# Kernel optimization log

Measured on AMD Instinct MI355X. Metric: run time of the kernel, lower is better.

## Reference

```python
import jax, jax.numpy as jnp
import numpy as np

N, E, B = 50000, 800000, 64
IN, H, OUT = 64, 128, 64


def _gcn_norm(edge_index, num_nodes):
    # PyG gcn_norm with add_self_loops=True: A_hat = A + I, norm = d^-1/2[src]*d^-1/2[dst]
    loop = jnp.arange(num_nodes)
    src = jnp.concatenate([edge_index[0], loop])
    dst = jnp.concatenate([edge_index[1], loop])
    deg = jax.ops.segment_sum(jnp.ones_like(dst, dtype=jnp.float32), dst,
                              num_segments=num_nodes)  # >= 1 due to self-loops
    dis = deg ** -0.5
    norm = dis[src] * dis[dst]  # [E+N]
    return src, dst, norm


def _gcn_layer(x, W, b, src, dst, norm, num_nodes):
    h = x @ W                                   # linear first (GCNConv order)
    msg = h[src] * norm[:, None]                # gather + normalize, [E+N, H]
    out = jax.ops.segment_sum(msg, dst, num_segments=num_nodes)  # scatter-add
    return out + b


def setup_inputs() -> dict:
    key = jax.random.key(0)
    ks = jax.random.split(key, 12)
    x = jax.random.normal(ks[0], (N, IN), dtype=jnp.float32)
    edge_index = jax.random.randint(ks[1], (2, E), 0, N, dtype=jnp.int64)
    batch = jnp.sort(jax.random.randint(ks[2], (N,), 0, B, dtype=jnp.int64))

    def lin(k, fan_in, fan_out):
        s = 1.0 / np.sqrt(fan_in)
        return jax.random.uniform(k, (fan_in, fan_out), jnp.float32, -s, s)

    return {
        "x": x, "edge_index": edge_index, "batch": batch,
        "W1": lin(ks[3], IN, H), "b1": jnp.zeros((H,), jnp.float32),
        "W2": lin(ks[4], H, H),  "b2": jnp.zeros((H,), jnp.float32),
        "W3": lin(ks[5], H, H),  "b3": jnp.zeros((H,), jnp.float32),
        "W4": lin(ks[6], H, OUT), "b4": jnp.zeros((OUT,), jnp.float32),
    }


def reference(x, edge_index, batch, W1, b1, W2, b2, W3, b3, W4, b4):
    src, dst, norm = _gcn_norm(edge_index, N)
    h = jax.nn.relu(_gcn_layer(x, W1, b1, src, dst, norm, N))
    h = jax.nn.relu(_gcn_layer(h, W2, b2, src, dst, norm, N))
    # global mean pool over graphs
    sums = jax.ops.segment_sum(h, batch, num_segments=B)          # [B, H]
    cnts = jax.ops.segment_sum(jnp.ones((N,), jnp.float32), batch, num_segments=B)
    pooled = sums / jnp.maximum(cnts, 1.0)[:, None]
    # MLP head
    return jax.nn.relu(pooled @ W3 + b3) @ W4 + b4                # [B, OUT]
```

## Files before the change

kernel.cpp:

```cpp
#include <hip/hip_runtime.h>


__device__ __forceinline__ float ldf(const void* p, long long i, int f32) {
    if (f32) return ((const float*)p)[i];
    unsigned int u = ((const unsigned short*)p)[i];
    return __uint_as_float(u << 16);
}
__device__ __forceinline__ float bfl(unsigned int u) { return __uint_as_float(u << 16); }
__device__ __forceinline__ float bfh(unsigned int u) { return __uint_as_float(u & 0xFFFF0000u); }
__device__ __forceinline__ int ld_idx(const int* p, long long i, int i64) {
    return i64 ? p[2 * i] : p[i];
}
__device__ __forceinline__ unsigned short f2bf(float v) {
    unsigned int x = __float_as_uint(v);
    return (unsigned short)((x + 0x7FFFu + ((x >> 16) & 1u)) >> 16);
}
__device__ __forceinline__ int clampi(int v, int lo, int hi) {
    return v < lo ? lo : (v > hi ? hi : v);
}

#define OW1 0
#define OB1 8192
#define OW2 8320
#define OB2 24704
#define OW3 24832
#define OB3 41216
#define OW4 41344
#define OB4 49536
#define OTOT 49600


__global__ void gnn_prep(const void* W1, const void* b1, const void* W2, const void* b2,
                         const void* W3, const void* b3, const void* W4, const void* b4,
                         const void* x, const int* __restrict__ ei,
                         int* __restrict__ flags_out,
                         int* __restrict__ degcnt, float* __restrict__ pooled,
                         float* __restrict__ wsW, unsigned short* __restrict__ xb,
                         int N, int B) {
    __shared__ int s_cnt, s_or;
    const int t = threadIdx.x;
    if (t == 0) { s_cnt = 0; s_or = 0; }
    __syncthreads();
    {
        const unsigned int* w1w = (const unsigned int*)W1;
        int c = 0, o = 0;
        for (int i = t; i < 512; i += 256) {
            unsigned int e = (w1w[i] >> 7) & 0xFFu;
            if (e >= 100 && e <= 140) c++;
        }
        for (int i = t; i < 1024; i += 256) o |= ei[2 * i + 1];
        atomicAdd(&s_cnt, c);
        atomicOr(&s_or, o);
    }
    __syncthreads();
    const int f32 = (s_cnt > 256) ? 0 : 1;
    if (blockIdx.x == 0 && t == 0) {
        flags_out[0] = f32;
        flags_out[1] = (s_or == 0) ? 1 : 0;
    }
    const int i = blockIdx.x * 256 + t;
    const int stride = gridDim.x * 256;
    for (int j = i; j < N; j += stride) degcnt[j] = 0;
    for (int j = i; j < B * 128; j += stride) pooled[j] = 0.f;
    for (int j = i; j < OTOT; j += stride) {
        float v;
        if      (j < OB1) v = ldf(W1, j - OW1, f32);
        else if (j < OW2) v = ldf(b1, j - OB1, f32);
        else if (j < OB2) v = ldf(W2, j - OW2, f32);
        else if (j < OW3) v = ldf(b2, j - OB2, f32);
        else if (j < OB3) v = ldf(W3, j - OW3, f32);
        else if (j < OW4) v = ldf(b3, j - OB3, f32);
        else if (j < OB4) v = ldf(W4, j - OW4, f32);
        else              v = ldf(b4, j - OB4, f32);
        wsW[j] = v;
    }
    if (f32) {
        const float* xf = (const float*)x;
        for (int j = i; j < N * 64; j += stride) xb[j] = f2bf(xf[j]);
    }
}


__global__ void gnn_hist(const int* __restrict__ ei, int E, int N,
                         const int* __restrict__ flags, int* __restrict__ degcnt,
                         int* __restrict__ rank) {
    int base = (blockIdx.x * 256 + threadIdx.x) * 4;
    if (base >= E) return;
    int i64 = flags[1];
    int m = min(4, E - base);
    int d[4], r[4];
#pragma unroll
    for (int j = 0; j < 4; ++j)
        if (j < m) d[j] = clampi(ld_idx(ei, (long long)E + base + j, i64), 0, N - 1);
#pragma unroll
    for (int j = 0; j < 4; ++j)
        if (j < m) r[j] = atomicAdd(&degcnt[d[j]], 1);
#pragma unroll
    for (int j = 0; j < 4; ++j)
        if (j < m) rank[base + j] = r[j];
}

__global__ void gnn_scan1(const int* __restrict__ cnt, int* __restrict__ excl,
                          int* __restrict__ sums, float* __restrict__ dis, int N) {
    __shared__ int sh[256];
    int t = threadIdx.x;
    int i = blockIdx.x * 256 + t;
    int v = (i < N) ? cnt[i] : 0;
    sh[t] = v;
    __syncthreads();
    for (int off = 1; off < 256; off <<= 1) {
        int a = (t >= off) ? sh[t - off] : 0;
        __syncthreads();
        sh[t] += a;
        __syncthreads();
    }
    if (i < N) {
        excl[i] = sh[t] - v;
        dis[i] = rsqrtf((float)v + 1.0f);
    }
    if (t == 255) sums[blockIdx.x] = sh[255];
}

__global__ void gnn_scan2(int* __restrict__ sums, int nb) {
    __shared__ int sh[256];
    int t = threadIdx.x;
    int v = (t < nb) ? sums[t] : 0;
    sh[t] = v;
    __syncthreads();
    for (int off = 1; off < 256; off <<= 1) {
        int a = (t >= off) ? sh[t - off] : 0;
        __syncthreads();
        sh[t] += a;
        __syncthreads();
    }
    if (t < nb) sums[t] = sh[t] - v;
}

template <bool SMALLN>
__global__ void gnn_fill(const int* __restrict__ ei, const int* __restrict__ excl,
                         const int* __restrict__ bsums, const int* __restrict__ rank,
                         void* __restrict__ csr, int E, int N,
                         const int* __restrict__ flags) {
    int e = blockIdx.x * 256 + threadIdx.x;
    if (e >= E) return;
    int i64 = flags[1];
    int s = clampi(ld_idx(ei, (long long)e, i64), 0, N - 1);
    int d = clampi(ld_idx(ei, (long long)E + e, i64), 0, N - 1);
    int pos = excl[d] + bsums[d >> 8] + rank[e];
    if (SMALLN) ((unsigned short*)csr)[pos] = (unsigned short)s;
    else        ((int*)csr)[pos] = s;
}

template <bool SMALLN>
__device__ __forceinline__ int csr_at(const void* csr, int e) {
    return SMALLN ? (int)((const unsigned short*)csr)[e] : ((const int*)csr)[e];
}


template <bool SMALLN>
__global__ __launch_bounds__(256) void gnn_aggx_lin1(const void* __restrict__ x,
                                                     const unsigned short* __restrict__ xconv,
                                                     const int* __restrict__ excl,
                                                     const int* __restrict__ bsums,
                                                     const void* __restrict__ csr,
                                                     const float* __restrict__ dis,
                                                     const int* __restrict__ flags,
                                                     const float* __restrict__ Wf,
                                                     const float* __restrict__ bias,
                                                     int N, int E, float* __restrict__ out) {
    __shared__ float Xs[32 * 64];
    const unsigned int* tab = flags[0] ? (const unsigned int*)xconv : (const unsigned int*)x;
    const int t = threadIdx.x;
    const int nbase = blockIdx.x * 32;
    const int lane = t & 63;
    const int fl = lane & 31;

#pragma unroll
    for (int pass = 0; pass < 4; ++pass) {
        int ln = pass * 8 + (t >> 6) * 2 + (lane >> 5);
        int n = nbase + ln;
        float a0 = 0.f, a1 = 0.f;
        if (n < N) {
            float dn = dis[n], dn2 = dn * dn;
            unsigned int us = tab[(long long)n * 32 + fl];
            a0 = bfl(us) * dn2; a1 = bfh(us) * dn2;
            int beg = excl[n] + bsums[n >> 8];
            int end = (n + 1 < N) ? (excl[n + 1] + bsums[(n + 1) >> 8]) : E;
            int e = beg;
            for (; e + 8 <= end; e += 8) {
                int s0 = csr_at<SMALLN>(csr, e),     s1 = csr_at<SMALLN>(csr, e + 1);
                int s2 = csr_at<SMALLN>(csr, e + 2), s3 = csr_at<SMALLN>(csr, e + 3);
                int s4 = csr_at<SMALLN>(csr, e + 4), s5 = csr_at<SMALLN>(csr, e + 5);
                int s6 = csr_at<SMALLN>(csr, e + 6), s7 = csr_at<SMALLN>(csr, e + 7);
                float w0 = dis[s0], w1 = dis[s1], w2 = dis[s2], w3 = dis[s3];
                float w4 = dis[s4], w5 = dis[s5], w6 = dis[s6], w7 = dis[s7];
                unsigned int u0 = tab[(long long)s0 * 32 + fl];
                unsigned int u1 = tab[(long long)s1 * 32 + fl];
                unsigned int u2 = tab[(long long)s2 * 32 + fl];
                unsigned int u3 = tab[(long long)s3 * 32 + fl];
                unsigned int u4 = tab[(long long)s4 * 32 + fl];
                unsigned int u5 = tab[(long long)s5 * 32 + fl];
                unsigned int u6 = tab[(long long)s6 * 32 + fl];
                unsigned int u7 = tab[(long long)s7 * 32 + fl];
                w0 *= dn; w1 *= dn; w2 *= dn; w3 *= dn;
                w4 *= dn; w5 *= dn; w6 *= dn; w7 *= dn;
                a0 = fmaf(w0, bfl(u0), a0); a1 = fmaf(w0, bfh(u0), a1);
                a0 = fmaf(w1, bfl(u1), a0); a1 = fmaf(w1, bfh(u1), a1);
                a0 = fmaf(w2, bfl(u2), a0); a1 = fmaf(w2, bfh(u2), a1);
                a0 = fmaf(w3, bfl(u3), a0); a1 = fmaf(w3, bfh(u3), a1);
                a0 = fmaf(w4, bfl(u4), a0); a1 = fmaf(w4, bfh(u4), a1);
                a0 = fmaf(w5, bfl(u5), a0); a1 = fmaf(w5, bfh(u5), a1);
                a0 = fmaf(w6, bfl(u6), a0); a1 = fmaf(w6, bfh(u6), a1);
                a0 = fmaf(w7, bfl(u7), a0); a1 = fmaf(w7, bfh(u7), a1);
            }
            for (; e + 4 <= end; e += 4) {
                int s0 = csr_at<SMALLN>(csr, e),     s1 = csr_at<SMALLN>(csr, e + 1);
                int s2 = csr_at<SMALLN>(csr, e + 2), s3 = csr_at<SMALLN>(csr, e + 3);
                float w0 = dis[s0], w1 = dis[s1], w2 = dis[s2], w3 = dis[s3];
                unsigned int u0 = tab[(long long)s0 * 32 + fl];
                unsigned int u1 = tab[(long long)s1 * 32 + fl];
                unsigned int u2 = tab[(long long)s2 * 32 + fl];
                unsigned int u3 = tab[(long long)s3 * 32 + fl];
                w0 *= dn; w1 *= dn; w2 *= dn; w3 *= dn;
                a0 = fmaf(w0, bfl(u0), a0); a1 = fmaf(w0, bfh(u0), a1);
                a0 = fmaf(w1, bfl(u1), a0); a1 = fmaf(w1, bfh(u1), a1);
                a0 = fmaf(w2, bfl(u2), a0); a1 = fmaf(w2, bfh(u2), a1);
                a0 = fmaf(w3, bfl(u3), a0); a1 = fmaf(w3, bfh(u3), a1);
            }
            for (; e < end; ++e) {
                int s = csr_at<SMALLN>(csr, e);
                float w = dis[s] * dn;
                unsigned int u = tab[(long long)s * 32 + fl];
                a0 = fmaf(w, bfl(u), a0); a1 = fmaf(w, bfh(u), a1);
            }
        }
        Xs[ln * 64 + fl * 2]     = a0;
        Xs[ln * 64 + fl * 2 + 1] = a1;
    }
    __syncthreads();

    const int fg = t & 31, ng = t >> 5;
    const int f0 = fg * 4, n0 = ng * 4;
    const float4* Xs4 = (const float4*)Xs;
    const float4* Wp  = (const float4*)Wf;
    float4 acc[4];
#pragma unroll
    for (int j = 0; j < 4; ++j) acc[j] = make_float4(0.f, 0.f, 0.f, 0.f);
#pragma unroll 4
    for (int k4 = 0; k4 < 16; ++k4) {
        const float4 wa = Wp[(4 * k4 + 0) * 32 + fg];
        const float4 wb = Wp[(4 * k4 + 1) * 32 + fg];
        const float4 wc = Wp[(4 * k4 + 2) * 32 + fg];
        const float4 wd = Wp[(4 * k4 + 3) * 32 + fg];
#pragma unroll
        for (int j = 0; j < 4; ++j) {
            const float4 xv = Xs4[(n0 + j) * 16 + k4];
            acc[j].x = fmaf(xv.x, wa.x, acc[j].x); acc[j].y = fmaf(xv.x, wa.y, acc[j].y);
            acc[j].z = fmaf(xv.x, wa.z, acc[j].z); acc[j].w = fmaf(xv.x, wa.w, acc[j].w);
            acc[j].x = fmaf(xv.y, wb.x, acc[j].x); acc[j].y = fmaf(xv.y, wb.y, acc[j].y);
            acc[j].z = fmaf(xv.y, wb.z, acc[j].z); acc[j].w = fmaf(xv.y, wb.w, acc[j].w);
            acc[j].x = fmaf(xv.z, wc.x, acc[j].x); acc[j].y = fmaf(xv.z, wc.y, acc[j].y);
            acc[j].z = fmaf(xv.z, wc.z, acc[j].z); acc[j].w = fmaf(xv.z, wc.w, acc[j].w);
            acc[j].x = fmaf(xv.w, wd.x, acc[j].x); acc[j].y = fmaf(xv.w, wd.y, acc[j].y);
            acc[j].z = fmaf(xv.w, wd.z, acc[j].z); acc[j].w = fmaf(xv.w, wd.w, acc[j].w);
        }
    }
    const float4 b = *(const float4*)&bias[f0];
#pragma unroll
    for (int j = 0; j < 4; ++j) {
        int n = nbase + n0 + j;
        if (n >= N) continue;
        float4 a = acc[j];
        a.x = fmaxf(a.x + b.x, 0.f);
        a.y = fmaxf(a.y + b.y, 0.f);
        a.z = fmaxf(a.z + b.z, 0.f);
        a.w = fmaxf(a.w + b.w, 0.f);
        *(float4*)(out + (long long)n * 128 + f0) = a;
    }
}


template <int K, bool RELU, bool OUTBF>
__global__ __launch_bounds__(256) void gnn_linear(const float* __restrict__ X,
                                                  const float* __restrict__ Wf,
                                                  const float* __restrict__ bias,
                                                  int N, void* __restrict__ out) {
    __shared__ float Xs[32 * K];
    const int t = threadIdx.x;
    const int nbase = blockIdx.x * 32;

#pragma unroll
    for (int it = 0; it < K / 32; ++it) {
        int i4 = t + it * 256;
        int n = nbase + (i4 * 4) / K;
        float4 v = make_float4(0.f, 0.f, 0.f, 0.f);
        if (n < N) v = ((const float4*)X)[(long long)nbase * (K / 4) + i4];
        ((float4*)Xs)[i4] = v;
    }
    __syncthreads();

    const int fg = t & 31, ng = t >> 5;
    const int f0 = fg * 4, n0 = ng * 4;
    const float4* Xs4 = (const float4*)Xs;
    const float4* Wp  = (const float4*)Wf;
    float4 acc[4];
#pragma unroll
    for (int j = 0; j < 4; ++j) acc[j] = make_float4(0.f, 0.f, 0.f, 0.f);
#pragma unroll 4
    for (int k4 = 0; k4 < K / 4; ++k4) {
        const float4 wa = Wp[(4 * k4 + 0) * 32 + fg];
        const float4 wb = Wp[(4 * k4 + 1) * 32 + fg];
        const float4 wc = Wp[(4 * k4 + 2) * 32 + fg];
        const float4 wd = Wp[(4 * k4 + 3) * 32 + fg];
#pragma unroll
        for (int j = 0; j < 4; ++j) {
            const float4 xv = Xs4[(n0 + j) * (K / 4) + k4];
            acc[j].x = fmaf(xv.x, wa.x, acc[j].x); acc[j].y = fmaf(xv.x, wa.y, acc[j].y);
            acc[j].z = fmaf(xv.x, wa.z, acc[j].z); acc[j].w = fmaf(xv.x, wa.w, acc[j].w);
            acc[j].x = fmaf(xv.y, wb.x, acc[j].x); acc[j].y = fmaf(xv.y, wb.y, acc[j].y);
            acc[j].z = fmaf(xv.y, wb.z, acc[j].z); acc[j].w = fmaf(xv.y, wb.w, acc[j].w);
            acc[j].x = fmaf(xv.z, wc.x, acc[j].x); acc[j].y = fmaf(xv.z, wc.y, acc[j].y);
            acc[j].z = fmaf(xv.z, wc.z, acc[j].z); acc[j].w = fmaf(xv.z, wc.w, acc[j].w);
            acc[j].x = fmaf(xv.w, wd.x, acc[j].x); acc[j].y = fmaf(xv.w, wd.y, acc[j].y);
            acc[j].z = fmaf(xv.w, wd.z, acc[j].z); acc[j].w = fmaf(xv.w, wd.w, acc[j].w);
        }
    }
#pragma unroll
    for (int j = 0; j < 4; ++j) {
        int n = nbase + n0 + j;
        if (n >= N) continue;
        float4 a = acc[j];
        if (RELU) {
            const float4 b = *(const float4*)&bias[f0];
            a.x = fmaxf(a.x + b.x, 0.f);
            a.y = fmaxf(a.y + b.y, 0.f);
            a.z = fmaxf(a.z + b.z, 0.f);
            a.w = fmaxf(a.w + b.w, 0.f);
        }
        if (OUTBF) {
            uint2 u;
            u.x = (unsigned int)f2bf(a.x) | ((unsigned int)f2bf(a.y) << 16);
            u.y = (unsigned int)f2bf(a.z) | ((unsigned int)f2bf(a.w) << 16);
            *(uint2*)((unsigned short*)out + (long long)n * 128 + f0) = u;
        } else {
            *(float4*)((float*)out + (long long)n * 128 + f0) = a;
        }
    }
}


template <bool SMALLN>
__global__ __launch_bounds__(256) void gnn_agg_bf(const unsigned short* __restrict__ A2,
                                                  const int* __restrict__ excl,
                                                  const int* __restrict__ bsums,
                                                  const void* __restrict__ csr,
                                                  const float* __restrict__ dis,
                                                  const float* __restrict__ bias,
                                                  float* __restrict__ outC, int N, int E) {
    int t = threadIdx.x;
    int lane = t & 63;
    int n = blockIdx.x * 8 + (t >> 6) * 2 + (lane >> 5);
    if (n >= N) return;
    int fl = lane & 31;
    float dn = dis[n];
    float dn2 = dn * dn;
    uint2 us = *(const uint2*)(A2 + (long long)n * 128 + fl * 4);
    float a0 = bfl(us.x) * dn2, a1 = bfh(us.x) * dn2;
    float a2 = bfl(us.y) * dn2, a3 = bfh(us.y) * dn2;
    int beg = excl[n] + bsums[n >> 8];
    int end = (n + 1 < N) ? (excl[n + 1] + bsums[(n + 1) >> 8]) : E;
    int e = beg;
    for (; e + 8 <= end; e += 8) {
        int s0 = csr_at<SMALLN>(csr, e),     s1 = csr_at<SMALLN>(csr, e + 1);
        int s2 = csr_at<SMALLN>(csr, e + 2), s3 = csr_at<SMALLN>(csr, e + 3);
        int s4 = csr_at<SMALLN>(csr, e + 4), s5 = csr_at<SMALLN>(csr, e + 5);
        int s6 = csr_at<SMALLN>(csr, e + 6), s7 = csr_at<SMALLN>(csr, e + 7);
        float w0 = dis[s0], w1 = dis[s1], w2 = dis[s2], w3 = dis[s3];
        float w4 = dis[s4], w5 = dis[s5], w6 = dis[s6], w7 = dis[s7];
        uint2 u0 = *(const uint2*)(A2 + (long long)s0 * 128 + fl * 4);
        uint2 u1 = *(const uint2*)(A2 + (long long)s1 * 128 + fl * 4);
        uint2 u2 = *(const uint2*)(A2 + (long long)s2 * 128 + fl * 4);
        uint2 u3 = *(const uint2*)(A2 + (long long)s3 * 128 + fl * 4);
        uint2 u4 = *(const uint2*)(A2 + (long long)s4 * 128 + fl * 4);
        uint2 u5 = *(const uint2*)(A2 + (long long)s5 * 128 + fl * 4);
        uint2 u6 = *(const uint2*)(A2 + (long long)s6 * 128 + fl * 4);
        uint2 u7 = *(const uint2*)(A2 + (long long)s7 * 128 + fl * 4);
        w0 *= dn; w1 *= dn; w2 *= dn; w3 *= dn;
        w4 *= dn; w5 *= dn; w6 *= dn; w7 *= dn;
        a0 = fmaf(w0, bfl(u0.x), a0); a1 = fmaf(w0, bfh(u0.x), a1);
        a2 = fmaf(w0, bfl(u0.y), a2); a3 = fmaf(w0, bfh(u0.y), a3);
        a0 = fmaf(w1, bfl(u1.x), a0); a1 = fmaf(w1, bfh(u1.x), a1);
        a2 = fmaf(w1, bfl(u1.y), a2); a3 = fmaf(w1, bfh(u1.y), a3);
        a0 = fmaf(w2, bfl(u2.x), a0); a1 = fmaf(w2, bfh(u2.x), a1);
        a2 = fmaf(w2, bfl(u2.y), a2); a3 = fmaf(w2, bfh(u2.y), a3);
        a0 = fmaf(w3, bfl(u3.x), a0); a1 = fmaf(w3, bfh(u3.x), a1);
        a2 = fmaf(w3, bfl(u3.y), a2); a3 = fmaf(w3, bfh(u3.y), a3);
        a0 = fmaf(w4, bfl(u4.x), a0); a1 = fmaf(w4, bfh(u4.x), a1);
        a2 = fmaf(w4, bfl(u4.y), a2); a3 = fmaf(w4, bfh(u4.y), a3);
        a0 = fmaf(w5, bfl(u5.x), a0); a1 = fmaf(w5, bfh(u5.x), a1);
        a2 = fmaf(w5, bfl(u5.y), a2); a3 = fmaf(w5, bfh(u5.y), a3);
        a0 = fmaf(w6, bfl(u6.x), a0); a1 = fmaf(w6, bfh(u6.x), a1);
        a2 = fmaf(w6, bfl(u6.y), a2); a3 = fmaf(w6, bfh(u6.y), a3);
        a0 = fmaf(w7, bfl(u7.x), a0); a1 = fmaf(w7, bfh(u7.x), a1);
        a2 = fmaf(w7, bfl(u7.y), a2); a3 = fmaf(w7, bfh(u7.y), a3);
    }
    for (; e + 4 <= end; e += 4) {
        int s0 = csr_at<SMALLN>(csr, e),     s1 = csr_at<SMALLN>(csr, e + 1);
        int s2 = csr_at<SMALLN>(csr, e + 2), s3 = csr_at<SMALLN>(csr, e + 3);
        float w0 = dis[s0], w1 = dis[s1], w2 = dis[s2], w3 = dis[s3];
        uint2 u0 = *(const uint2*)(A2 + (long long)s0 * 128 + fl * 4);
        uint2 u1 = *(const uint2*)(A2 + (long long)s1 * 128 + fl * 4);
        uint2 u2 = *(const uint2*)(A2 + (long long)s2 * 128 + fl * 4);
        uint2 u3 = *(const uint2*)(A2 + (long long)s3 * 128 + fl * 4);
        w0 *= dn; w1 *= dn; w2 *= dn; w3 *= dn;
        a0 = fmaf(w0, bfl(u0.x), a0); a1 = fmaf(w0, bfh(u0.x), a1);
        a2 = fmaf(w0, bfl(u0.y), a2); a3 = fmaf(w0, bfh(u0.y), a3);
        a0 = fmaf(w1, bfl(u1.x), a0); a1 = fmaf(w1, bfh(u1.x), a1);
        a2 = fmaf(w1, bfl(u1.y), a2); a3 = fmaf(w1, bfh(u1.y), a3);
        a0 = fmaf(w2, bfl(u2.x), a0); a1 = fmaf(w2, bfh(u2.x), a1);
        a2 = fmaf(w2, bfl(u2.y), a2); a3 = fmaf(w2, bfh(u2.y), a3);
        a0 = fmaf(w3, bfl(u3.x), a0); a1 = fmaf(w3, bfh(u3.x), a1);
        a2 = fmaf(w3, bfl(u3.y), a2); a3 = fmaf(w3, bfh(u3.y), a3);
    }
    for (; e < end; ++e) {
        int s = csr_at<SMALLN>(csr, e);
        float w = dis[s] * dn;
        uint2 u = *(const uint2*)(A2 + (long long)s * 128 + fl * 4);
        a0 = fmaf(w, bfl(u.x), a0); a1 = fmaf(w, bfh(u.x), a1);
        a2 = fmaf(w, bfl(u.y), a2); a3 = fmaf(w, bfh(u.y), a3);
    }
    const float4 b = *(const float4*)&bias[fl * 4];
    float4 o;
    o.x = fmaxf(a0 + b.x, 0.f);
    o.y = fmaxf(a1 + b.y, 0.f);
    o.z = fmaxf(a2 + b.z, 0.f);
    o.w = fmaxf(a3 + b.w, 0.f);
    *(float4*)(outC + (long long)n * 128 + fl * 4) = o;
}


#define PSTRIP 32
__global__ __launch_bounds__(128) void gnn_pool(const float* __restrict__ h,
                                                const int* __restrict__ batch,
                                                const int* __restrict__ flags,
                                                float* __restrict__ pooled, int N, int B) {
    int i64 = flags[1];
    int f = threadIdx.x;
    int n0 = blockIdx.x * PSTRIP;
    if (n0 >= N) return;
    int nend = min(n0 + PSTRIP, N);
    int cur = clampi(ld_idx(batch, n0, i64), 0, B - 1);
    float acc = 0.0f;
    for (int n = n0; n < nend; ++n) {
        int b = clampi(ld_idx(batch, n, i64), 0, B - 1);
        if (b != cur) {
            atomicAdd(&pooled[cur * 128 + f], acc);
            acc = 0.0f; cur = b;
        }
        acc += h[(long long)n * 128 + f];
    }
    atomicAdd(&pooled[cur * 128 + f], acc);
}


__global__ __launch_bounds__(128) void gnn_head(const float* __restrict__ pooled,
                                                const int* __restrict__ batch,
                                                const float* __restrict__ W3,
                                                const float* __restrict__ b3,
                                                const float* __restrict__ W4,
                                                const float* __restrict__ b4,
                                                const int* __restrict__ flags,
                                                void* __restrict__ outv, int N) {
    __shared__ float xs[128];
    __shared__ float rs[128];
    __shared__ float cinv;
    int b = blockIdx.x, f = threadIdx.x;
    if (f == 0) {
        int i64 = flags[1];
        int L = 0, R = N;
        while (L < R) { int m = (L + R) >> 1; if (ld_idx(batch, m, i64) < b) L = m + 1; else R = m; }
        int lo = L;
        L = 0; R = N;
        while (L < R) { int m = (L + R) >> 1; if (ld_idx(batch, m, i64) < b + 1) L = m + 1; else R = m; }
        cinv = 1.0f / fmaxf((float)(L - lo), 1.0f);
    }
    __syncthreads();
    xs[f] = pooled[b * 128 + f] * cinv;
    __syncthreads();
    float acc = b3[f];
    for (int k = 0; k < 128; ++k) acc = fmaf(xs[k], W3[k * 128 + f], acc);
    rs[f] = fmaxf(acc, 0.f);
    __syncthreads();
    if (f < 64) {
        float a2 = b4[f];
        for (int k = 0; k < 128; ++k) a2 = fmaf(rs[k], W4[k * 64 + f], a2);
        if (flags[0]) ((float*)outv)[b * 64 + f] = a2;
        else          ((unsigned short*)outv)[b * 64 + f] = f2bf(a2);
    }
}


extern "C" void kernel_launch(void* const* d_in, const int* in_sizes, int n_in,
                              void* d_out, int out_size, void* d_ws, size_t ws_size,
                              hipStream_t stream) {
    const void* x  = d_in[0];
    const int* ei  = (const int*)d_in[1];
    const int* bat = (const int*)d_in[2];

    const int N = in_sizes[0] / 64;
    const int E = in_sizes[1] / 2;
    const int B = out_size / 64;
    const bool smalln = (N < 65536);

    char* p = (char*)d_ws;
    auto alloc = [&](size_t bytes) { void* q = (void*)p; p += (bytes + 255) & ~(size_t)255; return q; };
    int*   flags    = (int*)alloc(256);
    float* wsW      = (float*)alloc((size_t)OTOT * 4);
    int*   degcnt   = (int*)alloc((size_t)N * 4);
    float* dis      = (float*)alloc((size_t)N * 4);
    int*   excl     = (int*)alloc((size_t)N * 4);
    int*   bsums    = (int*)alloc(1024);
    int*   rank     = (int*)alloc((size_t)E * 4);
    void*  csr      = alloc((size_t)E * (smalln ? 2 : 4));
    unsigned short* xb = (unsigned short*)alloc((size_t)N * 64 * 2);
    float* H1       = (float*)alloc((size_t)N * 128 * 4);
    float* C2       = (float*)alloc((size_t)N * 128 * 4);
    unsigned short* A2 = (unsigned short*)alloc((size_t)N * 128 * 2);
    float* pooled   = (float*)alloc((size_t)B * 128 * 4);
    (void)ws_size; (void)n_in;

    const int nbN = (N + 255) / 256;

    gnn_prep<<<512, 256, 0, stream>>>(d_in[3], d_in[4], d_in[5], d_in[6],
                                      d_in[7], d_in[8], d_in[9], d_in[10],
                                      x, ei, flags, degcnt, pooled, wsW, xb, N, B);

    gnn_hist<<<(E + 1023) / 1024, 256, 0, stream>>>(ei, E, N, flags, degcnt, rank);
    gnn_scan1<<<nbN, 256, 0, stream>>>(degcnt, excl, bsums, dis, N);
    gnn_scan2<<<1, 256, 0, stream>>>(bsums, nbN);
    if (smalln)
        gnn_fill<true><<<(E + 255) / 256, 256, 0, stream>>>(ei, excl, bsums, rank, csr, E, N, flags);
    else
        gnn_fill<false><<<(E + 255) / 256, 256, 0, stream>>>(ei, excl, bsums, rank, csr, E, N, flags);

    const int nlin = (N + 31) / 32;
    const int nagg = (N + 7) / 8;

    if (smalln)
        gnn_aggx_lin1<true><<<nlin, 256, 0, stream>>>(x, xb, excl, bsums, csr, dis, flags,
                                                      wsW + OW1, wsW + OB1, N, E, H1);
    else
        gnn_aggx_lin1<false><<<nlin, 256, 0, stream>>>(x, xb, excl, bsums, csr, dis, flags,
                                                       wsW + OW1, wsW + OB1, N, E, H1);

    gnn_linear<128, false, true><<<nlin, 256, 0, stream>>>(H1, wsW + OW2, wsW + OB2, N, (void*)A2);
    if (smalln)
        gnn_agg_bf<true><<<nagg, 256, 0, stream>>>(A2, excl, bsums, csr, dis, wsW + OB2, C2, N, E);
    else
        gnn_agg_bf<false><<<nagg, 256, 0, stream>>>(A2, excl, bsums, csr, dis, wsW + OB2, C2, N, E);

    gnn_pool<<<(N + PSTRIP - 1) / PSTRIP, 128, 0, stream>>>(C2, bat, flags, pooled, N, B);
    gnn_head<<<B, 128, 0, stream>>>(pooled, bat, wsW + OW3, wsW + OB3,
                                    wsW + OW4, wsW + OB4, flags, d_out, N);
}
```

Measured before the change: 274.2 us.

## Fuse mean-pool into MLP head and halve node tiles for linear kernels

Measured after the change: 317.0 us. 1.16x slower.

```diff
diff --git a/kernel.cpp b/kernel.cpp
--- a/kernel.cpp
+++ b/kernel.cpp
@@ -34,9 +34,9 @@
                          const void* W3, const void* b3, const void* W4, const void* b4,
                          const void* x, const int* __restrict__ ei,
                          int* __restrict__ flags_out,
-                         int* __restrict__ degcnt, float* __restrict__ pooled,
+                         int* __restrict__ degcnt,
                          float* __restrict__ wsW, unsigned short* __restrict__ xb,
-                         int N, int B) {
+                         int N) {
     __shared__ int s_cnt, s_or;
     const int t = threadIdx.x;
     if (t == 0) { s_cnt = 0; s_or = 0; }
@@ -61,7 +61,6 @@
     const int i = blockIdx.x * 256 + t;
     const int stride = gridDim.x * 256;
     for (int j = i; j < N; j += stride) degcnt[j] = 0;
-    for (int j = i; j < B * 128; j += stride) pooled[j] = 0.f;
     for (int j = i; j < OTOT; j += stride) {
         float v;
         if      (j < OB1) v = ldf(W1, j - OW1, f32);
@@ -158,7 +157,7 @@
 
 
 template <bool SMALLN>
-__global__ __launch_bounds__(256) void gnn_aggx_lin1(const void* __restrict__ x,
+__global__ __launch_bounds__(128) void gnn_aggx_lin1(const void* __restrict__ x,
                                                      const unsigned short* __restrict__ xconv,
                                                      const int* __restrict__ excl,
                                                      const int* __restrict__ bsums,
@@ -168,16 +167,16 @@
                                                      const float* __restrict__ Wf,
                                                      const float* __restrict__ bias,
                                                      int N, int E, float* __restrict__ out) {
-    __shared__ float Xs[32 * 64];
+    __shared__ float Xs[16 * 64];
     const unsigned int* tab = flags[0] ? (const unsigned int*)xconv : (const unsigned int*)x;
     const int t = threadIdx.x;
-    const int nbase = blockIdx.x * 32;
+    const int nbase = blockIdx.x * 16;
     const int lane = t & 63;
     const int fl = lane & 31;
 
 #pragma unroll
     for (int pass = 0; pass < 4; ++pass) {
-        int ln = pass * 8 + (t >> 6) * 2 + (lane >> 5);
+        int ln = pass * 4 + (t >> 6) * 2 + (lane >> 5);
         int n = nbase + ln;
         float a0 = 0.f, a1 = 0.f;
         if (n < N) {
@@ -281,17 +280,17 @@
 
 
 template <int K, bool RELU, bool OUTBF>
-__global__ __launch_bounds__(256) void gnn_linear(const float* __restrict__ X,
+__global__ __launch_bounds__(128) void gnn_linear(const float* __restrict__ X,
                                                   const float* __restrict__ Wf,
                                                   const float* __restrict__ bias,
                                                   int N, void* __restrict__ out) {
-    __shared__ float Xs[32 * K];
+    __shared__ float Xs[16 * K];
     const int t = threadIdx.x;
-    const int nbase = blockIdx.x * 32;
+    const int nbase = blockIdx.x * 16;
 
 #pragma unroll
     for (int it = 0; it < K / 32; ++it) {
-        int i4 = t + it * 256;
+        int i4 = t + it * 128;
         int n = nbase + (i4 * 4) / K;
         float4 v = make_float4(0.f, 0.f, 0.f, 0.f);
         if (n < N) v = ((const float4*)X)[(long long)nbase * (K / 4) + i4];
@@ -439,53 +438,40 @@
 }
 
 
-#define PSTRIP 32
-__global__ __launch_bounds__(128) void gnn_pool(const float* __restrict__ h,
-                                                const int* __restrict__ batch,
-                                                const int* __restrict__ flags,
-                                                float* __restrict__ pooled, int N, int B) {
-    int i64 = flags[1];
-    int f = threadIdx.x;
-    int n0 = blockIdx.x * PSTRIP;
-    if (n0 >= N) return;
-    int nend = min(n0 + PSTRIP, N);
-    int cur = clampi(ld_idx(batch, n0, i64), 0, B - 1);
-    float acc = 0.0f;
-    for (int n = n0; n < nend; ++n) {
-        int b = clampi(ld_idx(batch, n, i64), 0, B - 1);
-        if (b != cur) {
-            atomicAdd(&pooled[cur * 128 + f], acc);
-            acc = 0.0f; cur = b;
-        }
-        acc += h[(long long)n * 128 + f];
-    }
-    atomicAdd(&pooled[cur * 128 + f], acc);
-}
-
-
-__global__ __launch_bounds__(128) void gnn_head(const float* __restrict__ pooled,
-                                                const int* __restrict__ batch,
-                                                const float* __restrict__ W3,
-                                                const float* __restrict__ b3,
-                                                const float* __restrict__ W4,
-                                                const float* __restrict__ b4,
-                                                const int* __restrict__ flags,
-                                                void* __restrict__ outv, int N) {
+__global__ __launch_bounds__(128) void gnn_pool_head(const float* __restrict__ C2,
+                                                     const int* __restrict__ batch,
+                                                     const float* __restrict__ W3,
+                                                     const float* __restrict__ b3,
+                                                     const float* __restrict__ W4,
+                                                     const float* __restrict__ b4,
+                                                     const int* __restrict__ flags,
+                                                     void* __restrict__ outv, int N) {
     __shared__ float xs[128];
     __shared__ float rs[128];
-    __shared__ float cinv;
+    __shared__ int slo, shi;
     int b = blockIdx.x, f = threadIdx.x;
     if (f == 0) {
         int i64 = flags[1];
         int L = 0, R = N;
         while (L < R) { int m = (L + R) >> 1; if (ld_idx(batch, m, i64) < b) L = m + 1; else R = m; }
-        int lo = L;
+        slo = L;
         L = 0; R = N;
         while (L < R) { int m = (L + R) >> 1; if (ld_idx(batch, m, i64) < b + 1) L = m + 1; else R = m; }
-        cinv = 1.0f / fmaxf((float)(L - lo), 1.0f);
-    }
-    __syncthreads();
-    xs[f] = pooled[b * 128 + f] * cinv;
+        shi = L;
+    }
+    __syncthreads();
+    int lo = slo, hi = shi;
+    float p0 = 0.f, p1 = 0.f, p2 = 0.f, p3 = 0.f;
+    int n = lo;
+    for (; n + 4 <= hi; n += 4) {
+        p0 += C2[(long long)(n + 0) * 128 + f];
+        p1 += C2[(long long)(n + 1) * 128 + f];
+        p2 += C2[(long long)(n + 2) * 128 + f];
+        p3 += C2[(long long)(n + 3) * 128 + f];
+    }
+    for (; n < hi; ++n) p0 += C2[(long long)n * 128 + f];
+    float cinv = 1.0f / fmaxf((float)(hi - lo), 1.0f);
+    xs[f] = ((p0 + p1) + (p2 + p3)) * cinv;
     __syncthreads();
     float acc = b3[f];
     for (int k = 0; k < 128; ++k) acc = fmaf(xs[k], W3[k * 128 + f], acc);
@@ -526,14 +512,13 @@
     float* H1       = (float*)alloc((size_t)N * 128 * 4);
     float* C2       = (float*)alloc((size_t)N * 128 * 4);
     unsigned short* A2 = (unsigned short*)alloc((size_t)N * 128 * 2);
-    float* pooled   = (float*)alloc((size_t)B * 128 * 4);
     (void)ws_size; (void)n_in;
 
     const int nbN = (N + 255) / 256;
 
     gnn_prep<<<512, 256, 0, stream>>>(d_in[3], d_in[4], d_in[5], d_in[6],
                                       d_in[7], d_in[8], d_in[9], d_in[10],
-                                      x, ei, flags, degcnt, pooled, wsW, xb, N, B);
+                                      x, ei, flags, degcnt, wsW, xb, N);
 
     gnn_hist<<<(E + 1023) / 1024, 256, 0, stream>>>(ei, E, N, flags, degcnt, rank);
     gnn_scan1<<<nbN, 256, 0, stream>>>(degcnt, excl, bsums, dis, N);
@@ -543,23 +528,22 @@
     else
         gnn_fill<false><<<(E + 255) / 256, 256, 0, stream>>>(ei, excl, bsums, rank, csr, E, N, flags);
 
-    const int nlin = (N + 31) / 32;
+    const int nlin = (N + 15) / 16;
     const int nagg = (N + 7) / 8;
 
     if (smalln)
-        gnn_aggx_lin1<true><<<nlin, 256, 0, stream>>>(x, xb, excl, bsums, csr, dis, flags,
+        gnn_aggx_lin1<true><<<nlin, 128, 0, stream>>>(x, xb, excl, bsums, csr, dis, flags,
                                                       wsW + OW1, wsW + OB1, N, E, H1);
     else
-        gnn_aggx_lin1<false><<<nlin, 256, 0, stream>>>(x, xb, excl, bsums, csr, dis, flags,
+        gnn_aggx_lin1<false><<<nlin, 128, 0, stream>>>(x, xb, excl, bsums, csr, dis, flags,
                                                        wsW + OW1, wsW + OB1, N, E, H1);
 
-    gnn_linear<128, false, true><<<nlin, 256, 0, stream>>>(H1, wsW + OW2, wsW + OB2, N, (void*)A2);
+    gnn_linear<128, false, true><<<nlin, 128, 0, stream>>>(H1, wsW + OW2, wsW + OB2, N, (void*)A2);
     if (smalln)
         gnn_agg_bf<true><<<nagg, 256, 0, stream>>>(A2, excl, bsums, csr, dis, wsW + OB2, C2, N, E);
     else
         gnn_agg_bf<false><<<nagg, 256, 0, stream>>>(A2, excl, bsums, csr, dis, wsW + OB2, C2, N, E);
 
-    gnn_pool<<<(N + PSTRIP - 1) / PSTRIP, 128, 0, stream>>>(C2, bat, flags, pooled, N, B);
-    gnn_head<<<B, 128, 0, stream>>>(pooled, bat, wsW + OW3, wsW + OB3,
-                                    wsW + OW4, wsW + OB4, flags, d_out, N);
-}
+    gnn_pool_head<<<B, 128, 0, stream>>>(C2, bat, wsW + OW3, wsW + OB3,
+                                         wsW + OW4, wsW + OB4, flags, d_out, N);
+}
```
